# Optimization experiments

Measured on AMD Instinct MI355X. Metric: run time of the kernel, lower is better.

Reference implementation:

```python
import jax, jax.numpy as jnp
import numpy as np

B, S, D_MODEL, D_FF, N_EXPERTS, TOP_K = 4, 4096, 512, 2048, 8, 2


def setup_inputs() -> dict:
    key = jax.random.key(0)
    k1, k2, k3, k4 = jax.random.split(key, 4)
    hidden_states = jax.random.normal(k1, (B, S, D_MODEL), dtype=jnp.float32)
    gate_w = jax.random.normal(k2, (N_EXPERTS, D_MODEL), dtype=jnp.float32) * 0.02
    w1 = jax.random.normal(k3, (N_EXPERTS, D_FF, D_MODEL), dtype=jnp.float32) * (1.0 / np.sqrt(D_MODEL))
    w2 = jax.random.normal(k4, (N_EXPERTS, D_MODEL, D_FF), dtype=jnp.float32) * 0.02
    return {"hidden_states": hidden_states, "gate_w": gate_w, "w1": w1, "w2": w2}


def reference(hidden_states, gate_w, w1, w2):
    b, s, d = hidden_states.shape
    t = b * s
    n_experts = w1.shape[0]
    flat = hidden_states.reshape(t, d)                         # [T, D]

    # Router
    router_logits = flat @ gate_w.T                            # [T, E]
    routing_probs = jax.nn.softmax(router_logits, axis=-1)
    routing_weights, selected_experts = jax.lax.top_k(routing_probs, TOP_K)
    routing_weights = routing_weights / routing_weights.sum(axis=-1, keepdims=True)

    # Dense all-expert FFN (eval mode: dropout is identity). GELU exact (erf), as nn.GELU default.
    h = jax.nn.gelu(jnp.einsum('td,efd->tef', flat, w1), approximate=False)  # [T, E, d_ff]
    expert_outputs = jnp.einsum('tef,egf->teg', h, w2)         # [T, E, D]

    # scatter_add routing weights into dense [T, E] matrix, then weighted combine
    ewm = jnp.zeros((t, n_experts), dtype=flat.dtype)
    ewm = ewm.at[jnp.arange(t)[:, None], selected_experts].add(routing_weights)
    combined = jnp.einsum('te,ted->td', ewm, expert_outputs)   # [T, D]
    output = combined.reshape(b, s, d)

    # entropy regularization loss
    log_probs = jnp.log(jnp.clip(routing_probs, 1e-6))
    entropy_loss = (-(routing_probs * log_probs).sum(axis=-1)).mean()

    return output, router_logits, entropy_loss
```

## Files before the change

kernel.cpp:

```cpp
#include <hip/hip_runtime.h>
#include <hip/hip_bf16.h>
#include <math.h>

#define T_TOKENS 16384
#define DM 512
#define DFF 2048
#define NE 8
#define TOKT 64
#define FCH 256
#define NFC (DFF / FCH)

#define RL_OFF  ((size_t)T_TOKENS * DM)
#define ENT_OFF (RL_OFF + (size_t)T_TOKENS * NE)

typedef __attribute__((ext_vector_type(8))) short short8;
typedef __attribute__((ext_vector_type(4))) float f32x4;

__device__ __forceinline__ unsigned short f2bf(float f) {
    union { float f; unsigned u; } v; v.f = f;
    unsigned r = v.u + 0x7FFFu + ((v.u >> 16) & 1u);
    return (unsigned short)(r >> 16);
}
__device__ __forceinline__ float bf2f(unsigned short h) {
    union { unsigned u; float f; } v; v.u = ((unsigned)h) << 16; return v.f;
}
__device__ __forceinline__ void atomAddF(float* p, float v) {
    __hip_atomic_fetch_add(p, v, __ATOMIC_RELAXED, __HIP_MEMORY_SCOPE_AGENT);
}

__global__ void cvt_kernel(const float* __restrict__ src, unsigned short* __restrict__ dst, size_t n4) {
    for (size_t i = blockIdx.x * (size_t)blockDim.x + threadIdx.x; i < n4;
         i += (size_t)gridDim.x * blockDim.x) {
        f32x4 v = ((const f32x4*)src)[i];
        unsigned short b0 = f2bf(v.x), b1 = f2bf(v.y), b2 = f2bf(v.z), b3 = f2bf(v.w);
        ((unsigned long long*)dst)[i] =
            (unsigned long long)b0 | ((unsigned long long)b1 << 16) |
            ((unsigned long long)b2 << 32) | ((unsigned long long)b3 << 48);
    }
}

__global__ __launch_bounds__(1024)
void router_kernel(const float* __restrict__ x, const float* __restrict__ gw,
                   float* __restrict__ out, int* __restrict__ cursor,
                   int* __restrict__ slotlist, float* __restrict__ wgtlist,
                   float* __restrict__ entPartial) {
    __shared__ int   lcnt[NE];
    __shared__ int   lbase[NE];
    __shared__ float lent[16];
    __shared__ int   le[16][2];
    __shared__ int   lpos[16][2];
    __shared__ float lw[16][2];

    int tid = threadIdx.x;
    int wid = tid >> 6, lane = tid & 63;
    int t = blockIdx.x * 16 + wid;
    if (tid < NE) lcnt[tid] = 0;
    __syncthreads();

    const float* xr = x + (size_t)t * DM + lane * 8;
    f32x4 x0 = *(const f32x4*)xr;
    f32x4 x1 = *(const f32x4*)(xr + 4);

    float logit[NE];
#pragma unroll
    for (int e = 0; e < NE; ++e) {
        const float* g = gw + e * DM + lane * 8;
        f32x4 g0 = *(const f32x4*)g;
        f32x4 g1 = *(const f32x4*)(g + 4);
        float p = x0.x*g0.x + x0.y*g0.y + x0.z*g0.z + x0.w*g0.w
                + x1.x*g1.x + x1.y*g1.y + x1.z*g1.z + x1.w*g1.w;
#pragma unroll
        for (int off = 32; off > 0; off >>= 1) p += __shfl_xor(p, off);
        logit[e] = p;
    }
    float m = logit[0];
#pragma unroll
    for (int e = 1; e < NE; ++e) m = fmaxf(m, logit[e]);
    float pr[NE]; float s = 0.f;
#pragma unroll
    for (int e = 0; e < NE; ++e) { pr[e] = expf(logit[e] - m); s += pr[e]; }
    float inv = 1.f / s;
    float ent = 0.f;
#pragma unroll
    for (int e = 0; e < NE; ++e) { pr[e] *= inv; ent -= pr[e] * logf(fmaxf(pr[e], 1e-6f)); }
    float p0 = -1.f, p1 = -1.f; int e0 = 0, e1 = 0;
#pragma unroll
    for (int e = 0; e < NE; ++e) {
        float p = pr[e];
        if (p > p0)      { p1 = p0; e1 = e0; p0 = p; e0 = e; }
        else if (p > p1) { p1 = p;  e1 = e; }
    }
    float wsum = p0 + p1;

    if (lane == 0) {
        lent[wid] = ent;
        le[wid][0] = e0; le[wid][1] = e1;
        lw[wid][0] = p0 / wsum; lw[wid][1] = p1 / wsum;
        lpos[wid][0] = atomicAdd(&lcnt[e0], 1);
        lpos[wid][1] = atomicAdd(&lcnt[e1], 1);
    }
    float myLogit = 0.f;
#pragma unroll
    for (int e = 0; e < NE; ++e) if (lane == e) myLogit = logit[e];
    if (lane < NE) out[RL_OFF + (size_t)t * NE + lane] = myLogit;

    __syncthreads();
    if (tid < NE) lbase[tid] = atomicAdd(cursor + tid, lcnt[tid]);
    __syncthreads();
    if (tid < 16) {
        int a0 = le[tid][0], a1 = le[tid][1];
        int tt = blockIdx.x * 16 + tid;
        int q0 = lbase[a0] + lpos[tid][0];
        int q1 = lbase[a1] + lpos[tid][1];
        slotlist[a0 * T_TOKENS + q0] = tt * 2;     wgtlist[a0 * T_TOKENS + q0] = lw[tid][0];
        slotlist[a1 * T_TOKENS + q1] = tt * 2 + 1; wgtlist[a1 * T_TOKENS + q1] = lw[tid][1];
    }
    if (tid == 0) {
        float sum = 0.f;
#pragma unroll
        for (int w = 0; w < 16; ++w) sum += lent[w];
        entPartial[blockIdx.x] = sum;
    }
}

__global__ void ent_reduce(const float* __restrict__ part, float* __restrict__ out) {
    __shared__ float s[16];
    int tid = threadIdx.x;
    float v = part[tid];
#pragma unroll
    for (int off = 32; off > 0; off >>= 1) v += __shfl_xor(v, off);
    if ((tid & 63) == 0) s[tid >> 6] = v;
    __syncthreads();
    if (tid == 0) {
        float tot = 0.f;
#pragma unroll
        for (int w = 0; w < 16; ++w) tot += s[w];
        out[ENT_OFF] = tot * (1.0f / T_TOKENS);
    }
}

template <int XB, int SLOT>
__global__ __launch_bounds__(512, 2)
void ffn_kernel(const float* __restrict__ x, const unsigned short* __restrict__ xb,
                const unsigned short* __restrict__ w1b, const unsigned short* __restrict__ w2b,
                const int* __restrict__ cursor, const int* __restrict__ slotlist,
                const float* __restrict__ wgtlist,
                unsigned short* __restrict__ ybuf, float* __restrict__ out) {
    __shared__ char XsB[TOKT * DM * 2];
    __shared__ char HsB[TOKT * FCH * 2];
    __shared__ int   tIdx[TOKT];
    __shared__ float tW[TOKT];

    int e   = blockIdx.x & 7;
    int cnt = cursor[e];
    int tid = threadIdx.x;
    int wid = tid >> 6, lane = tid & 63;
    int l16 = lane & 15, lg = lane >> 4;
    int swz = (l16 & 7) << 4;

    const unsigned short* w1e = w1b + (size_t)e * DFF * DM;
    const unsigned short* w2e = w2b + (size_t)e * DM * DFF;
    const int*   sl = slotlist + e * T_TOKENS;
    const float* wl = wgtlist  + e * T_TOKENS;

    int step = (gridDim.x >> 3) * TOKT;
#pragma unroll 1
    for (int t0 = (blockIdx.x >> 3) * TOKT; t0 < cnt; t0 += step) {
        if (tid < TOKT) {
            int i = t0 + tid;
            int src = (i < cnt) ? i : t0;
            tIdx[tid] = sl[src] >> 1;
            tW[tid]   = (i < cnt) ? wl[i] : 0.f;
        }
#pragma unroll
        for (int it = 0; it < 8; ++it) {
            int u = tid + it * 512;
            int row = u >> 6, c16 = u & 63;
            int idx = t0 + row;
            int sidx = (idx < cnt) ? idx : t0;
            int t = sl[sidx] >> 1;
            short8 v;
            if constexpr (XB == 1) {
                v = *(const short8*)(xb + (size_t)t * DM + c16 * 8);
            } else {
                const float* src = x + (size_t)t * DM + c16 * 8;
                f32x4 a = *(const f32x4*)src, b = *(const f32x4*)(src + 4);
                v[0]=(short)f2bf(a.x); v[1]=(short)f2bf(a.y); v[2]=(short)f2bf(a.z); v[3]=(short)f2bf(a.w);
                v[4]=(short)f2bf(b.x); v[5]=(short)f2bf(b.y); v[6]=(short)f2bf(b.z); v[7]=(short)f2bf(b.w);
            }
            *(short8*)(XsB + row * 1024 + ((c16 << 4) ^ ((row & 7) << 4))) = v;
        }
        __syncthreads();

        f32x4 Yacc[4][4] = {};
        const unsigned short* w1base = w1e + (size_t)(wid * 32 + l16) * DM + lg * 8;
        const unsigned short* w2base = w2e + (size_t)(wid * 64 + l16) * DFF + lg * 8;

        short8 Ap[3][2];
#pragma unroll
        for (int k = 0; k < 3; ++k) {
            Ap[k][0] = *(const short8*)(w1base + k * 32);
            Ap[k][1] = *(const short8*)(w1base + 16 * DM + k * 32);
        }

#pragma unroll 1
        for (int fc = 0; fc < NFC; ++fc) {
            const unsigned short* w1f = w1base + (size_t)fc * FCH * DM;
            f32x4 Hacc[2][4] = {};
#pragma unroll
            for (int ks = 0; ks < 16; ++ks) {
                short8 a0 = Ap[ks % 3][0], a1 = Ap[ks % 3][1];
                if (ks < 13) {
                    Ap[ks % 3][0] = *(const short8*)(w1f + (ks + 3) * 32);
                    Ap[ks % 3][1] = *(const short8*)(w1f + 16 * DM + (ks + 3) * 32);
                }
#pragma unroll
                for (int tt = 0; tt < 4; ++tt) {
                    short8 xf = *(const short8*)(XsB + (tt * 16 + l16) * 1024 +
                                                 ((ks * 64 + lg * 16) ^ swz));
                    Hacc[0][tt] = __builtin_amdgcn_mfma_f32_16x16x32_bf16(a0, xf, Hacc[0][tt], 0, 0, 0);
                    Hacc[1][tt] = __builtin_amdgcn_mfma_f32_16x16x32_bf16(a1, xf, Hacc[1][tt], 0, 0, 0);
                }
            }
            if (fc + 1 < NFC) {
                const unsigned short* w1n = w1base + (size_t)(fc + 1) * FCH * DM;
#pragma unroll
                for (int k = 0; k < 3; ++k) {
                    Ap[k][0] = *(const short8*)(w1n + k * 32);
                    Ap[k][1] = *(const short8*)(w1n + 16 * DM + k * 32);
                }
            }
            const unsigned short* w2f = w2base + fc * FCH;
            short8 Bp[2][4];
#pragma unroll
            for (int k = 0; k < 2; ++k)
#pragma unroll
                for (int gt = 0; gt < 4; ++gt)
                    Bp[k][gt] = *(const short8*)(w2f + (size_t)gt * 16 * DFF + k * 32);

            __syncthreads();
#pragma unroll
            for (int ft = 0; ft < 2; ++ft)
#pragma unroll
            for (int tt = 0; tt < 4; ++tt) {
                f32x4 h = Hacc[ft][tt];
                unsigned long long pk = 0;
#pragma unroll
                for (int r = 0; r < 4; ++r) {
                    float g = 0.5f * h[r] * (1.0f + erff(h[r] * 0.70710678118f));
                    pk |= (unsigned long long)f2bf(g) << (r * 16);
                }
                int token = tt * 16 + l16;
                int f2 = wid * 64 + ft * 32 + lg * 8;
                *(unsigned long long*)(HsB + token * 512 + (f2 ^ swz)) = pk;
            }
            __syncthreads();
#pragma unroll
            for (int ks = 0; ks < 8; ++ks) {
                short8 b0 = Bp[ks & 1][0], b1 = Bp[ks & 1][1];
                short8 b2 = Bp[ks & 1][2], b3 = Bp[ks & 1][3];
                if (ks < 6) {
#pragma unroll
                    for (int gt = 0; gt < 4; ++gt)
                        Bp[ks & 1][gt] = *(const short8*)(w2f + (size_t)gt * 16 * DFF + (ks + 2) * 32);
                }
#pragma unroll
                for (int tt = 0; tt < 4; ++tt) {
                    short8 af = *(const short8*)(HsB + (tt * 16 + l16) * 512 +
                                                 ((ks * 64 + lg * 16) ^ swz));
                    Yacc[tt][0] = __builtin_amdgcn_mfma_f32_16x16x32_bf16(af, b0, Yacc[tt][0], 0, 0, 0);
                    Yacc[tt][1] = __builtin_amdgcn_mfma_f32_16x16x32_bf16(af, b1, Yacc[tt][1], 0, 0, 0);
                    Yacc[tt][2] = __builtin_amdgcn_mfma_f32_16x16x32_bf16(af, b2, Yacc[tt][2], 0, 0, 0);
                    Yacc[tt][3] = __builtin_amdgcn_mfma_f32_16x16x32_bf16(af, b3, Yacc[tt][3], 0, 0, 0);
                }
            }
        }
#pragma unroll
        for (int tt = 0; tt < 4; ++tt)
#pragma unroll
        for (int r = 0; r < 4; ++r) {
            int row = tt * 16 + lg * 4 + r;
            int idx = t0 + row;
            if (idx < cnt) {
                int entry = sl[idx];
                float wgt = tW[row];
                if constexpr (SLOT == 1) {
                    unsigned short* dst = ybuf + (size_t)entry * DM + wid * 64;
#pragma unroll
                    for (int gt = 0; gt < 4; ++gt)
                        dst[gt * 16 + l16] = f2bf(Yacc[tt][gt][r] * wgt);
                } else {
                    float* dst = out + (size_t)(entry >> 1) * DM + wid * 64;
#pragma unroll
                    for (int gt = 0; gt < 4; ++gt)
                        atomAddF(dst + gt * 16 + l16, Yacc[tt][gt][r] * wgt);
                }
            }
        }
        __syncthreads();
    }
}

__global__ __launch_bounds__(256)
void combine_kernel(const unsigned short* __restrict__ ybuf, float* __restrict__ out) {
    int gid = blockIdx.x * 256 + threadIdx.x;
    int t = gid >> 6, c8 = (gid & 63) * 8;
    const unsigned short* r0 = ybuf + ((size_t)t * 2) * DM + c8;
    short8 a = *(const short8*)r0;
    short8 b = *(const short8*)(r0 + DM);
    float* o = out + (size_t)t * DM + c8;
    f32x4 v0, v1;
    v0.x = bf2f((unsigned short)a[0]) + bf2f((unsigned short)b[0]);
    v0.y = bf2f((unsigned short)a[1]) + bf2f((unsigned short)b[1]);
    v0.z = bf2f((unsigned short)a[2]) + bf2f((unsigned short)b[2]);
    v0.w = bf2f((unsigned short)a[3]) + bf2f((unsigned short)b[3]);
    v1.x = bf2f((unsigned short)a[4]) + bf2f((unsigned short)b[4]);
    v1.y = bf2f((unsigned short)a[5]) + bf2f((unsigned short)b[5]);
    v1.z = bf2f((unsigned short)a[6]) + bf2f((unsigned short)b[6]);
    v1.w = bf2f((unsigned short)a[7]) + bf2f((unsigned short)b[7]);
    *(f32x4*)o = v0;
    *(f32x4*)(o + 4) = v1;
}

extern "C" void kernel_launch(void* const* d_in, const int* in_sizes, int n_in,
                              void* d_out, int out_size, void* d_ws, size_t ws_size,
                              hipStream_t stream) {
    const float* x  = (const float*)d_in[0];
    const float* gw = (const float*)d_in[1];
    const float* w1 = (const float*)d_in[2];
    const float* w2 = (const float*)d_in[3];
    float* out = (float*)d_out;
    char* ws = (char*)d_ws;

    const size_t W1N = (size_t)NE * DFF * DM;
    const size_t W2N = (size_t)NE * DM * DFF;
    unsigned short* w1b = (unsigned short*)ws;
    unsigned short* w2b = w1b + W1N;
    size_t off = (W1N + W2N) * 2;
    int*   cursor   = (int*)(ws + off);   off += 256;
    int*   slotlist = (int*)(ws + off);   off += (size_t)NE * T_TOKENS * 4;
    float* wgtlist  = (float*)(ws + off); off += (size_t)NE * T_TOKENS * 4;
    float* entPart  = (float*)(ws + off); off += 8192;
    unsigned short* xbb = (unsigned short*)(ws + off); off += (size_t)T_TOKENS * DM * 2;
    size_t needB = off;
    unsigned short* ybuf = (unsigned short*)(ws + off); off += (size_t)T_TOKENS * 2 * DM * 2;
    size_t needA = off;

    int tier = (ws_size >= needA) ? 2 : ((ws_size >= needB) ? 1 : 0);

    hipMemsetAsync(cursor, 0, 64, stream);
    if (tier < 2) hipMemsetAsync(out, 0, RL_OFF * sizeof(float), stream);

    cvt_kernel<<<2048, 256, 0, stream>>>(w1, w1b, W1N / 4);
    cvt_kernel<<<2048, 256, 0, stream>>>(w2, w2b, W2N / 4);
    if (tier >= 1) cvt_kernel<<<2048, 256, 0, stream>>>(x, xbb, (size_t)T_TOKENS * DM / 4);

    router_kernel<<<T_TOKENS / 16, 1024, 0, stream>>>(x, gw, out, cursor, slotlist, wgtlist, entPart);
    ent_reduce<<<1, 1024, 0, stream>>>(entPart, out);

    if (tier == 2) {
        ffn_kernel<1, 1><<<NE * 64, 512, 0, stream>>>(x, xbb, w1b, w2b, cursor, slotlist, wgtlist, ybuf, out);
        combine_kernel<<<(T_TOKENS * DM / 8) / 256, 256, 0, stream>>>(ybuf, out);
    } else if (tier == 1) {
        ffn_kernel<1, 0><<<NE * 64, 512, 0, stream>>>(x, xbb, w1b, w2b, cursor, slotlist, wgtlist, nullptr, out);
    } else {
        ffn_kernel<0, 0><<<NE * 64, 512, 0, stream>>>(x, nullptr, w1b, w2b, cursor, slotlist, wgtlist, nullptr, out);
    }
}
```

Measured before the change: 515.1 us.

## Stream X in double-buffered K-chunks via direct global-to-LDS loads, raise occupancy

The FFN kernel no longer stages the full 64x512 bf16 token tile in LDS. It streams 128-wide K chunks into a double buffer with global_load_lds, which shrinks LDS use so launch bounds can move from 2 to 4 blocks. W1/W2 register prefetch pipelines are replaced with direct per-step loads, relying on occupancy to hide latency instead. The x-to-bf16 conversion is folded into the router kernel, removing one conversion launch. Risks are more register pressure at 4 waves/SIMD, extra barriers per chunk, and re-gathering X rows once per fc chunk.

```diff
diff --git a/kernel.cpp b/kernel.cpp
--- a/kernel.cpp
+++ b/kernel.cpp
@@ -9,6 +9,8 @@
 #define TOKT 64
 #define FCH 256
 #define NFC (DFF / FCH)
+#define KCH 128
+#define NKC (DM / KCH)
 
 #define RL_OFF  ((size_t)T_TOKENS * DM)
 #define ENT_OFF (RL_OFF + (size_t)T_TOKENS * NE)
@@ -26,6 +28,13 @@
 }
 __device__ __forceinline__ void atomAddF(float* p, float v) {
     __hip_atomic_fetch_add(p, v, __ATOMIC_RELAXED, __HIP_MEMORY_SCOPE_AGENT);
+}
+
+__device__ __forceinline__ void gl16(const void* g, void* l) {
+    __builtin_amdgcn_global_load_lds(
+        (const __attribute__((address_space(1))) unsigned*)(unsigned long long)g,
+        (__attribute__((address_space(3))) unsigned*)(unsigned)(unsigned long long)l,
+        16, 0, 0);
 }
 
 __global__ void cvt_kernel(const float* __restrict__ src, unsigned short* __restrict__ dst, size_t n4) {
@@ -43,7 +52,7 @@
 void router_kernel(const float* __restrict__ x, const float* __restrict__ gw,
                    float* __restrict__ out, int* __restrict__ cursor,
                    int* __restrict__ slotlist, float* __restrict__ wgtlist,
-                   float* __restrict__ entPartial) {
+                   float* __restrict__ entPartial, unsigned short* __restrict__ xbw) {
     __shared__ int   lcnt[NE];
     __shared__ int   lbase[NE];
     __shared__ float lent[16];
@@ -60,6 +69,13 @@
     const float* xr = x + (size_t)t * DM + lane * 8;
     f32x4 x0 = *(const f32x4*)xr;
     f32x4 x1 = *(const f32x4*)(xr + 4);
+
+    if (xbw) {
+        short8 v;
+        v[0]=(short)f2bf(x0.x); v[1]=(short)f2bf(x0.y); v[2]=(short)f2bf(x0.z); v[3]=(short)f2bf(x0.w);
+        v[4]=(short)f2bf(x1.x); v[5]=(short)f2bf(x1.y); v[6]=(short)f2bf(x1.z); v[7]=(short)f2bf(x1.w);
+        *(short8*)(xbw + (size_t)t * DM + lane * 8) = v;
+    }
 
     float logit[NE];
 #pragma unroll
@@ -140,16 +156,14 @@
 }
 
 template <int XB, int SLOT>
-__global__ __launch_bounds__(512, 2)
+__global__ __launch_bounds__(512, 4)
 void ffn_kernel(const float* __restrict__ x, const unsigned short* __restrict__ xb,
                 const unsigned short* __restrict__ w1b, const unsigned short* __restrict__ w2b,
                 const int* __restrict__ cursor, const int* __restrict__ slotlist,
                 const float* __restrict__ wgtlist,
                 unsigned short* __restrict__ ybuf, float* __restrict__ out) {
-    __shared__ char XsB[TOKT * DM * 2];
+    __shared__ char XcB[2][TOKT * KCH * 2];
     __shared__ char HsB[TOKT * FCH * 2];
-    __shared__ int   tIdx[TOKT];
-    __shared__ float tW[TOKT];
 
     int e   = blockIdx.x & 7;
     int cnt = cursor[e];
@@ -163,82 +177,80 @@
     const int*   sl = slotlist + e * T_TOKENS;
     const float* wl = wgtlist  + e * T_TOKENS;
 
+    int srow = (wid << 2) + (lane >> 4);
+    int slot = lane & 15;
     int step = (gridDim.x >> 3) * TOKT;
+
 #pragma unroll 1
     for (int t0 = (blockIdx.x >> 3) * TOKT; t0 < cnt; t0 += step) {
-        if (tid < TOKT) {
-            int i = t0 + tid;
-            int src = (i < cnt) ? i : t0;
-            tIdx[tid] = sl[src] >> 1;
-            tW[tid]   = (i < cnt) ? wl[i] : 0.f;
-        }
-#pragma unroll
-        for (int it = 0; it < 8; ++it) {
-            int u = tid + it * 512;
-            int row = u >> 6, c16 = u & 63;
-            int idx = t0 + row;
-            int sidx = (idx < cnt) ? idx : t0;
-            int t = sl[sidx] >> 1;
-            short8 v;
-            if constexpr (XB == 1) {
-                v = *(const short8*)(xb + (size_t)t * DM + c16 * 8);
-            } else {
-                const float* src = x + (size_t)t * DM + c16 * 8;
-                f32x4 a = *(const f32x4*)src, b = *(const f32x4*)(src + 4);
+        int i0 = t0 + srow, i1 = i0 + 32;
+        int tok0 = sl[(i0 < cnt) ? i0 : t0] >> 1;
+        int tok1 = sl[(i1 < cnt) ? i1 : t0] >> 1;
+        const unsigned short* s0 = xb + (size_t)tok0 * DM + ((slot ^ (srow & 7)) << 3);
+        const unsigned short* s1 = xb + (size_t)tok1 * DM + ((slot ^ (srow & 7)) << 3);
+        const float* xf0 = x + (size_t)tok0 * DM + (slot << 3);
+        const float* xf1 = x + (size_t)tok1 * DM + (slot << 3);
+
+        if constexpr (XB == 1) {
+            gl16(s0, XcB[0] + (wid << 10));
+            gl16(s1, XcB[0] + (wid << 10) + 8192);
+        } else {
+#pragma unroll
+            for (int u = 0; u < 2; ++u) {
+                int row = srow + u * 32;
+                const float* sp = (u ? xf1 : xf0);
+                f32x4 a = *(const f32x4*)sp, b = *(const f32x4*)(sp + 4);
+                short8 v;
                 v[0]=(short)f2bf(a.x); v[1]=(short)f2bf(a.y); v[2]=(short)f2bf(a.z); v[3]=(short)f2bf(a.w);
                 v[4]=(short)f2bf(b.x); v[5]=(short)f2bf(b.y); v[6]=(short)f2bf(b.z); v[7]=(short)f2bf(b.w);
-            }
-            *(short8*)(XsB + row * 1024 + ((c16 << 4) ^ ((row & 7) << 4))) = v;
+                *(short8*)(XcB[0] + row * 256 + ((slot << 4) ^ ((row & 7) << 4))) = v;
+            }
         }
         __syncthreads();
 
         f32x4 Yacc[4][4] = {};
-        const unsigned short* w1base = w1e + (size_t)(wid * 32 + l16) * DM + lg * 8;
-        const unsigned short* w2base = w2e + (size_t)(wid * 64 + l16) * DFF + lg * 8;
-
-        short8 Ap[3][2];
-#pragma unroll
-        for (int k = 0; k < 3; ++k) {
-            Ap[k][0] = *(const short8*)(w1base + k * 32);
-            Ap[k][1] = *(const short8*)(w1base + 16 * DM + k * 32);
-        }
 
 #pragma unroll 1
         for (int fc = 0; fc < NFC; ++fc) {
-            const unsigned short* w1f = w1base + (size_t)fc * FCH * DM;
             f32x4 Hacc[2][4] = {};
 #pragma unroll
-            for (int ks = 0; ks < 16; ++ks) {
-                short8 a0 = Ap[ks % 3][0], a1 = Ap[ks % 3][1];
-                if (ks < 13) {
-                    Ap[ks % 3][0] = *(const short8*)(w1f + (ks + 3) * 32);
-                    Ap[ks % 3][1] = *(const short8*)(w1f + 16 * DM + (ks + 3) * 32);
-                }
-#pragma unroll
-                for (int tt = 0; tt < 4; ++tt) {
-                    short8 xf = *(const short8*)(XsB + (tt * 16 + l16) * 1024 +
-                                                 ((ks * 64 + lg * 16) ^ swz));
-                    Hacc[0][tt] = __builtin_amdgcn_mfma_f32_16x16x32_bf16(a0, xf, Hacc[0][tt], 0, 0, 0);
-                    Hacc[1][tt] = __builtin_amdgcn_mfma_f32_16x16x32_bf16(a1, xf, Hacc[1][tt], 0, 0, 0);
-                }
-            }
-            if (fc + 1 < NFC) {
-                const unsigned short* w1n = w1base + (size_t)(fc + 1) * FCH * DM;
-#pragma unroll
-                for (int k = 0; k < 3; ++k) {
-                    Ap[k][0] = *(const short8*)(w1n + k * 32);
-                    Ap[k][1] = *(const short8*)(w1n + 16 * DM + k * 32);
-                }
-            }
-            const unsigned short* w2f = w2base + fc * FCH;
-            short8 Bp[2][4];
-#pragma unroll
-            for (int k = 0; k < 2; ++k)
-#pragma unroll
-                for (int gt = 0; gt < 4; ++gt)
-                    Bp[k][gt] = *(const short8*)(w2f + (size_t)gt * 16 * DFF + k * 32);
-
-            __syncthreads();
+            for (int kc = 0; kc < NKC; ++kc) {
+                char* rbuf = XcB[kc & 1];
+                char* wbuf = XcB[(kc & 1) ^ 1];
+                if (kc < NKC - 1 || fc < NFC - 1) {
+                    int nkc = (kc + 1) & 3;
+                    if constexpr (XB == 1) {
+                        gl16(s0 + nkc * KCH, wbuf + (wid << 10));
+                        gl16(s1 + nkc * KCH, wbuf + (wid << 10) + 8192);
+                    } else {
+#pragma unroll
+                        for (int u = 0; u < 2; ++u) {
+                            int row = srow + u * 32;
+                            const float* sp = (u ? xf1 : xf0) + nkc * KCH;
+                            f32x4 a = *(const f32x4*)sp, b = *(const f32x4*)(sp + 4);
+                            short8 v;
+                            v[0]=(short)f2bf(a.x); v[1]=(short)f2bf(a.y); v[2]=(short)f2bf(a.z); v[3]=(short)f2bf(a.w);
+                            v[4]=(short)f2bf(b.x); v[5]=(short)f2bf(b.y); v[6]=(short)f2bf(b.z); v[7]=(short)f2bf(b.w);
+                            *(short8*)(wbuf + row * 256 + ((slot << 4) ^ ((row & 7) << 4))) = v;
+                        }
+                    }
+                }
+                const unsigned short* w1p = w1e + (size_t)(fc * FCH + wid * 32 + l16) * DM
+                                            + kc * KCH + lg * 8;
+#pragma unroll
+                for (int ks = 0; ks < 4; ++ks) {
+                    short8 a0 = *(const short8*)(w1p + ks * 32);
+                    short8 a1 = *(const short8*)(w1p + 16 * DM + ks * 32);
+#pragma unroll
+                    for (int tt = 0; tt < 4; ++tt) {
+                        int row = tt * 16 + l16;
+                        short8 xfr = *(const short8*)(rbuf + row * 256 + ((ks * 64 + lg * 16) ^ swz));
+                        Hacc[0][tt] = __builtin_amdgcn_mfma_f32_16x16x32_bf16(a0, xfr, Hacc[0][tt], 0, 0, 0);
+                        Hacc[1][tt] = __builtin_amdgcn_mfma_f32_16x16x32_bf16(a1, xfr, Hacc[1][tt], 0, 0, 0);
+                    }
+                }
+                __syncthreads();
+            }
 #pragma unroll
             for (int ft = 0; ft < 2; ++ft)
 #pragma unroll
@@ -255,19 +267,17 @@
                 *(unsigned long long*)(HsB + token * 512 + (f2 ^ swz)) = pk;
             }
             __syncthreads();
+            const unsigned short* w2p = w2e + (size_t)(wid * 64 + l16) * DFF + fc * FCH + lg * 8;
 #pragma unroll
             for (int ks = 0; ks < 8; ++ks) {
-                short8 b0 = Bp[ks & 1][0], b1 = Bp[ks & 1][1];
-                short8 b2 = Bp[ks & 1][2], b3 = Bp[ks & 1][3];
-                if (ks < 6) {
-#pragma unroll
-                    for (int gt = 0; gt < 4; ++gt)
-                        Bp[ks & 1][gt] = *(const short8*)(w2f + (size_t)gt * 16 * DFF + (ks + 2) * 32);
-                }
+                short8 b0 = *(const short8*)(w2p + ks * 32);
+                short8 b1 = *(const short8*)(w2p + (size_t)16 * DFF + ks * 32);
+                short8 b2 = *(const short8*)(w2p + (size_t)32 * DFF + ks * 32);
+                short8 b3 = *(const short8*)(w2p + (size_t)48 * DFF + ks * 32);
 #pragma unroll
                 for (int tt = 0; tt < 4; ++tt) {
-                    short8 af = *(const short8*)(HsB + (tt * 16 + l16) * 512 +
-                                                 ((ks * 64 + lg * 16) ^ swz));
+                    int row = tt * 16 + l16;
+                    short8 af = *(const short8*)(HsB + row * 512 + ((ks * 64 + lg * 16) ^ swz));
                     Yacc[tt][0] = __builtin_amdgcn_mfma_f32_16x16x32_bf16(af, b0, Yacc[tt][0], 0, 0, 0);
                     Yacc[tt][1] = __builtin_amdgcn_mfma_f32_16x16x32_bf16(af, b1, Yacc[tt][1], 0, 0, 0);
                     Yacc[tt][2] = __builtin_amdgcn_mfma_f32_16x16x32_bf16(af, b2, Yacc[tt][2], 0, 0, 0);
@@ -283,7 +293,7 @@
             int idx = t0 + row;
             if (idx < cnt) {
                 int entry = sl[idx];
-                float wgt = tW[row];
+                float wgt = wl[idx];
                 if constexpr (SLOT == 1) {
                     unsigned short* dst = ybuf + (size_t)entry * DM + wid * 64;
 #pragma unroll
@@ -297,7 +307,6 @@
                 }
             }
         }
-        __syncthreads();
     }
 }
 
@@ -353,9 +362,9 @@
 
     cvt_kernel<<<2048, 256, 0, stream>>>(w1, w1b, W1N / 4);
     cvt_kernel<<<2048, 256, 0, stream>>>(w2, w2b, W2N / 4);
-    if (tier >= 1) cvt_kernel<<<2048, 256, 0, stream>>>(x, xbb, (size_t)T_TOKENS * DM / 4);
-
-    router_kernel<<<T_TOKENS / 16, 1024, 0, stream>>>(x, gw, out, cursor, slotlist, wgtlist, entPart);
+
+    router_kernel<<<T_TOKENS / 16, 1024, 0, stream>>>(x, gw, out, cursor, slotlist, wgtlist,
+                                                      entPart, tier >= 1 ? xbb : nullptr);
     ent_reduce<<<1, 1024, 0, stream>>>(entPart, out);
 
     if (tier == 2) {
```

Measured after the change: 571.0 us. 1.11x slower.
